# Performance work log

Measured on AMD Instinct MI355X. Metric: run time of the kernel, lower is better.

## Reference

```python
import jax, jax.numpy as jnp
import numpy as np

B, S, D, H = 2, 2048, 1024, 16
DK = D // H
NEG = -1.0e9

def setup_inputs() -> dict:
    key = jax.random.key(0)
    ks = jax.random.split(key, 12)
    sc = 1.0 / np.sqrt(D)
    q = jax.random.normal(ks[0], (B, S, D), jnp.float32)
    k = jax.random.normal(ks[1], (B, S, D), jnp.float32)
    v = jax.random.normal(ks[2], (B, S, D), jnp.float32)
    # causal mask: True = masked (matches masked_fill(mask == True, -1e9))
    mask = jnp.broadcast_to(jnp.triu(jnp.ones((S, S), bool), k=1)[None, None], (B, 1, S, S))
    Wq = jax.random.normal(ks[3], (D, D), jnp.float32) * sc
    bq = jnp.zeros((D,), jnp.float32)
    Wk = jax.random.normal(ks[4], (D, D), jnp.float32) * sc
    bk = jnp.zeros((D,), jnp.float32)
    Wv = jax.random.normal(ks[5], (D, D), jnp.float32) * sc
    bv = jnp.zeros((D,), jnp.float32)
    Wo = jax.random.normal(ks[6], (D, D), jnp.float32) * sc
    bo = jnp.zeros((D,), jnp.float32)
    return {"q": q, "k": k, "v": v, "mask": mask,
            "Wq": Wq, "bq": bq, "Wk": Wk, "bk": bk,
            "Wv": Wv, "bv": bv, "Wo": Wo, "bo": bo}

def reference(q, k, v, mask, Wq, bq, Wk, bk, Wv, bv, Wo, bo):
    def split_heads(x):  # [B,S,D] -> [B,H,S,DK]
        return x.reshape(B, S, H, DK).transpose(0, 2, 1, 3)
    qh = split_heads(q @ Wq + bq)
    kh = split_heads(k @ Wk + bk)
    vh = split_heads(v @ Wv + bv)
    scores = jnp.einsum('bhqd,bhkd->bhqk', qh, kh) / np.sqrt(DK)
    scores = jnp.where(mask, NEG, scores)
    p = jax.nn.softmax(scores, axis=-1)
    out = jnp.einsum('bhqk,bhkd->bhqd', p, vh)  # [B,H,S,DK]
    out = out.transpose(0, 2, 1, 3).reshape(B, S, D)
    return out @ Wo + bo
```

## Files before the change

### kernel.cpp

```cpp
#include <hip/hip_runtime.h>

#define BB 2
#define SS 2048
#define DD 1024
#define HH 16
#define DKK 64

typedef __attribute__((ext_vector_type(8))) short short8;
typedef __attribute__((ext_vector_type(4))) float floatx4;

__device__ inline float bf2f(ushort u) {
    union { unsigned int i; float f; } x; x.i = ((unsigned int)u) << 16; return x.f;
}
__device__ inline ushort f2bf(float f) {
    union { float f; unsigned int i; } x; x.f = f;
    unsigned int r = x.i + 0x7fff + ((x.i >> 16) & 1);
    return (ushort)(r >> 16);
}
__device__ inline void async_cp16(const ushort* g, ushort* l) {
    __builtin_amdgcn_global_load_lds(
        (const __attribute__((address_space(1))) unsigned int*)g,
        (__attribute__((address_space(3))) unsigned int*)l, 16, 0, 0);
}
__device__ inline unsigned int cvt_pk_bf16(float lo, float hi) {
    unsigned int r;
    asm("v_cvt_pk_bf16_f32 %0, %1, %2" : "=v"(r) : "v"(lo), "v"(hi));
    return r;
}
__device__ inline void swap32(unsigned int& a, unsigned int& b) {
    asm("v_permlane32_swap_b32 %0, %1" : "+v"(a), "+v"(b));
}
__device__ inline void swap16(unsigned int& a, unsigned int& b) {
    asm("v_permlane16_swap_b32 %0, %1" : "+v"(a), "+v"(b));
}

__global__ __launch_bounds__(256) void cvt_w4(const float* __restrict__ w0,
                                              const float* __restrict__ w1,
                                              const float* __restrict__ w2,
                                              const float* __restrict__ w3,
                                              ushort* __restrict__ o0,
                                              ushort* __restrict__ o1,
                                              ushort* __restrict__ o2,
                                              ushort* __restrict__ o3) {
    __shared__ ushort t[32][33];
    int z = blockIdx.z;
    const float* in = (z == 0) ? w0 : (z == 1) ? w1 : (z == 2) ? w2 : w3;
    ushort* out = (z == 0) ? o0 : (z == 1) ? o1 : (z == 2) ? o2 : o3;
    int bx = blockIdx.x, by = blockIdx.y, tx = threadIdx.x;
    for (int i = threadIdx.y; i < 32; i += 8)
        t[i][tx] = f2bf(in[(size_t)(by * 32 + i) * DD + bx * 32 + tx]);
    __syncthreads();
    for (int i = threadIdx.y; i < 32; i += 8)
        out[(size_t)(bx * 32 + i) * DD + by * 32 + tx] = t[tx][i];
}

__global__ __launch_bounds__(256) void cvt_qkv(const float* __restrict__ q,
                                               const float* __restrict__ k,
                                               const float* __restrict__ v,
                                               ushort* __restrict__ oq,
                                               ushort* __restrict__ ok,
                                               ushort* __restrict__ ov) {
    int z = blockIdx.z;
    const float* in = (z == 0) ? q : (z == 1) ? k : v;
    ushort* out = (z == 0) ? oq : (z == 1) ? ok : ov;
    int i = blockIdx.x * 256 + threadIdx.x;
    float4 f0 = ((const float4*)in)[i * 2];
    float4 f1 = ((const float4*)in)[i * 2 + 1];
    short8 p;
    p[0] = (short)f2bf(f0.x); p[1] = (short)f2bf(f0.y);
    p[2] = (short)f2bf(f0.z); p[3] = (short)f2bf(f0.w);
    p[4] = (short)f2bf(f1.x); p[5] = (short)f2bf(f1.y);
    p[6] = (short)f2bf(f1.z); p[7] = (short)f2bf(f1.w);
    ((short8*)out)[i] = p;
}

__global__ __launch_bounds__(512, 2) void gemm_qkv(const ushort* __restrict__ Xq,
                                                   const ushort* __restrict__ Xk,
                                                   const ushort* __restrict__ Xv,
                                                   const ushort* __restrict__ WtQ,
                                                   const ushort* __restrict__ WtK,
                                                   const ushort* __restrict__ WtV,
                                                   const float* __restrict__ bq,
                                                   const float* __restrict__ bk,
                                                   const float* __restrict__ bv,
                                                   ushort* __restrict__ qh,
                                                   ushort* __restrict__ kh,
                                                   ushort* __restrict__ vt) {
    constexpr int K = 1024;
    constexpr int NKT = 32;
    __shared__ ushort smem[32768];

    int lin = blockIdx.x + (blockIdx.y << 2) + (blockIdx.z << 6);
    int wid = (lin & 7) * 24 + (lin >> 3);
    int z = wid >> 6;
    int rem = wid & 63;
    int byy = rem >> 2, bxx = rem & 3;
    int rowBase = byy * 256, colBase = bxx * 256;

    const ushort* Ag = (z == 0) ? Xq : (z == 1) ? Xk : Xv;
    const ushort* Bg = (z == 0) ? WtQ : (z == 1) ? WtK : WtV;
    const float* bias = (z == 0) ? bq : (z == 1) ? bk : bv;
    ushort* outp = (z == 0) ? qh : (z == 1) ? kh : vt;

    int tid = threadIdx.x;
    int wave = tid >> 6, lane = tid & 63, quad = lane >> 4, l15 = lane & 15;
    int wm = wave >> 2, wn = wave & 3;

    size_t srcA[2], srcB[2];
    int dstU[2];
#pragma unroll
    for (int r = 0; r < 2; ++r) {
        int lb = r * 8192 + wave * 1024 + lane * 16;
        int sl = lb ^ (((lb >> 9) & 1) << 5);
        int srow = sl >> 6;
        int scol = (sl & 63) >> 1;
        srcA[r] = (size_t)(rowBase + srow) * K + scol;
        srcB[r] = (size_t)(colBase + srow) * K + scol;
        dstU[r] = r * 4096 + wave * 512;
    }
    int aOff[2][4], bOff[4];
#pragma unroll
    for (int mh = 0; mh < 2; ++mh)
#pragma unroll
        for (int mi = 0; mi < 4; ++mi) {
            int row = wm * 128 + mh * 64 + mi * 16 + l15;
            aOff[mh][mi] = row * 32 + ((quad * 8) ^ (((row >> 3) & 1) << 4));
        }
#pragma unroll
    for (int ni = 0; ni < 4; ++ni) {
        int row = wn * 64 + ni * 16 + l15;
        bOff[ni] = 8192 + row * 32 + ((quad * 8) ^ (((row >> 3) & 1) << 4));
    }

    auto stageTile = [&](int u) {
        int slot = (u & 1) << 14;
        const ushort* As = Ag + u * 32;
        const ushort* Bs = Bg + u * 32;
        async_cp16(As + srcA[0], &smem[slot + dstU[0]]);
        async_cp16(As + srcA[1], &smem[slot + dstU[1]]);
        async_cp16(Bs + srcB[0], &smem[slot + 8192 + dstU[0]]);
        async_cp16(Bs + srcB[1], &smem[slot + 8192 + dstU[1]]);
    };

    floatx4 acc[8][4] = {};
    stageTile(0);
    for (int t = 0; t < NKT; ++t) {
        if (t < NKT - 1) {
            stageTile(t + 1);
            asm volatile("s_waitcnt vmcnt(4)" ::: "memory");
        } else {
            asm volatile("s_waitcnt vmcnt(0)" ::: "memory");
        }
        __builtin_amdgcn_s_barrier();
        __builtin_amdgcn_sched_barrier(0);
        int slot = (t & 1) << 14;
        short8 bfr[4];
#pragma unroll
        for (int ni = 0; ni < 4; ++ni)
            bfr[ni] = *(const short8*)&smem[slot + bOff[ni]];
#pragma unroll
        for (int mh = 0; mh < 2; ++mh) {
            short8 af[4];
#pragma unroll
            for (int mi = 0; mi < 4; ++mi)
                af[mi] = *(const short8*)&smem[slot + aOff[mh][mi]];
#pragma unroll
            for (int mi = 0; mi < 4; ++mi)
#pragma unroll
                for (int ni = 0; ni < 4; ++ni)
                    acc[mh * 4 + mi][ni] = __builtin_amdgcn_mfma_f32_16x16x32_bf16(
                        af[mi], bfr[ni], acc[mh * 4 + mi][ni], 0, 0, 0);
        }
        __builtin_amdgcn_sched_barrier(0);
        __builtin_amdgcn_s_barrier();
    }

    float bvv[4];
#pragma unroll
    for (int ni = 0; ni < 4; ++ni)
        bvv[ni] = bias[colBase + wn * 64 + ni * 16 + l15];
    if (z == 2) {
#pragma unroll
        for (int mi = 0; mi < 8; ++mi)
#pragma unroll
            for (int ni = 0; ni < 4; ++ni) {
                int col = colBase + wn * 64 + ni * 16 + l15;
                int h = col >> 6, dk = col & 63;
                int rowg = rowBase + wm * 128 + mi * 16 + quad * 4;
                int b = rowg >> 11, s = rowg & 2047;
                int2 v;
                v.x = (int)cvt_pk_bf16(acc[mi][ni][0] + bvv[ni], acc[mi][ni][1] + bvv[ni]);
                v.y = (int)cvt_pk_bf16(acc[mi][ni][2] + bvv[ni], acc[mi][ni][3] + bvv[ni]);
                *(int2*)&outp[((size_t)((b * HH + h) * DKK + dk)) * SS + s] = v;
            }
    } else {
#pragma unroll
        for (int mi = 0; mi < 8; ++mi)
#pragma unroll
            for (int ni = 0; ni < 4; ++ni) {
                int col = colBase + wn * 64 + ni * 16 + l15;
                int h = col >> 6, dk = col & 63;
#pragma unroll
                for (int i = 0; i < 4; ++i) {
                    int rowg = rowBase + wm * 128 + mi * 16 + quad * 4 + i;
                    int b = rowg >> 11, s = rowg & 2047;
                    outp[((size_t)((b * HH + h) * SS + s)) * DKK + dk] =
                        f2bf(acc[mi][ni][i] + bvv[ni]);
                }
            }
    }
}

__global__ __launch_bounds__(256) void gemm_fin(const ushort* __restrict__ A,
                                                const ushort* __restrict__ Bt,
                                                const float* __restrict__ bias,
                                                float* __restrict__ outp) {
    constexpr int K = 1024, N = 1024, NT = 32;
    __shared__ ushort smem[12288];
    int tid = threadIdx.x;
    int wave = tid >> 6, lane = tid & 63, quad = lane >> 4, l15 = lane & 15;
    int wm = wave >> 1, wn = wave & 1;

    int lin = blockIdx.x + (blockIdx.y << 3);
    int wid = (lin & 7) * 64 + (lin >> 3);
    int bx = wid & 7, by = wid >> 3;
    int rowBase = by * 64, colBase = bx * 128;

    auto stage = [&](int k0, int d) {
        int ab = d * 6144, bb2 = 2048 + d * 6144;
#pragma unroll
        for (int j = 0; j < 3; ++j) {
            int c = j * 4 + wave;
            int cbase = (c < 4) ? c * 64 : (c - 4) * 64;
            int cc = cbase + lane;
            int row = cc >> 2, sub = (cc & 3) * 8;
            if (c < 4)
                async_cp16(&A[(size_t)(rowBase + row) * K + k0 + sub], &smem[ab + cbase * 8]);
            else
                async_cp16(&Bt[(size_t)(colBase + row) * K + k0 + sub], &smem[bb2 + cbase * 8]);
        }
    };

    floatx4 acc[2][4] = {};
    stage(0, 0);
    __syncthreads();
    for (int t = 0; t < NT; ++t) {
        if (t + 1 < NT) stage((t + 1) * 32, (t + 1) & 1);
        int ab = (t & 1) * 6144, bb2 = 2048 + (t & 1) * 6144;
        short8 af[2], bf[4];
#pragma unroll
        for (int mi = 0; mi < 2; ++mi)
            af[mi] = *(const short8*)&smem[ab + (wm * 32 + mi * 16 + l15) * 32 + quad * 8];
#pragma unroll
        for (int ni = 0; ni < 4; ++ni)
            bf[ni] = *(const short8*)&smem[bb2 + (wn * 64 + ni * 16 + l15) * 32 + quad * 8];
#pragma unroll
        for (int mi = 0; mi < 2; ++mi)
#pragma unroll
            for (int ni = 0; ni < 4; ++ni)
                acc[mi][ni] = __builtin_amdgcn_mfma_f32_16x16x32_bf16(
                    af[mi], bf[ni], acc[mi][ni], 0, 0, 0);
        __syncthreads();
    }
    for (int mi = 0; mi < 2; ++mi)
        for (int ni = 0; ni < 4; ++ni) {
            int col = colBase + wn * 64 + ni * 16 + l15;
            float bv = bias[col];
            for (int i = 0; i < 4; ++i) {
                int row = rowBase + wm * 32 + mi * 16 + quad * 4 + i;
                outp[(size_t)row * N + col] = acc[mi][ni][i] + bv;
            }
        }
}

__global__ __launch_bounds__(256, 2) void flash_attn5(const ushort* __restrict__ qh,
                                                      const ushort* __restrict__ kh,
                                                      const ushort* __restrict__ vt,
                                                      ushort* __restrict__ attn) {
    constexpr int LD = 72;
    __shared__ ushort Ksm[2][64 * LD];
    __shared__ ushort Vsm[2][64 * LD];
    int tid = threadIdx.x;
    int h = blockIdx.y, b = blockIdx.z;
    int wave = tid >> 6, lane = tid & 63, quad = lane >> 4, l15 = lane & 15;
    const size_t headQK = ((size_t)(b * HH + h)) * SS * DKK;
    const size_t headV  = ((size_t)(b * HH + h)) * DKK * SS;
    int c0 = tid, r0 = c0 >> 3, s0 = (c0 & 7) * 8;
    int c1 = tid + 256, r1 = c1 >> 3, s1 = (c1 & 7) * 8;
    const int qt0 = blockIdx.x;
    const int qt1 = 31 - qt0;

    int qrow0 = qt0 * 64 + wave * 16 + l15;
    int qrow1 = qt1 * 64 + wave * 16 + l15;
    short8 q0a = *(const short8*)&qh[headQK + (size_t)qrow0 * DKK + quad * 8];
    short8 q0b = *(const short8*)&qh[headQK + (size_t)qrow0 * DKK + 32 + quad * 8];
    short8 q1a = *(const short8*)&qh[headQK + (size_t)qrow1 * DKK + quad * 8];
    short8 q1b = *(const short8*)&qh[headQK + (size_t)qrow1 * DKK + 32 + quad * 8];

    floatx4 o0[4] = {}, o1[4] = {};
    float l0 = 0.f, l1 = 0.f;
    int qsel = wave * 16 + l15;

    *(int4*)&Ksm[0][r0 * LD + s0] = *(const int4*)&kh[headQK + (size_t)r0 * DKK + s0];
    *(int4*)&Ksm[0][r1 * LD + s1] = *(const int4*)&kh[headQK + (size_t)r1 * DKK + s1];
    *(int4*)&Vsm[0][r0 * LD + s0] = *(const int4*)&vt[headV + (size_t)r0 * SS + s0];
    *(int4*)&Vsm[0][r1 * LD + s1] = *(const int4*)&vt[headV + (size_t)r1 * SS + s1];
    __syncthreads();

    for (int kt = 0; kt <= qt1; ++kt) {
        int cur = kt & 1;
        bool pre = (kt < qt1);
        bool act0 = (kt <= qt0);
        int4 kA, kB, vA, vB;
        if (pre) {
            const ushort* kp = &kh[headQK + (size_t)((kt + 1) * 64) * DKK];
            const ushort* vp = &vt[headV + (kt + 1) * 64];
            kA = *(const int4*)&kp[(size_t)r0 * DKK + s0];
            kB = *(const int4*)&kp[(size_t)r1 * DKK + s1];
            vA = *(const int4*)&vp[(size_t)r0 * SS + s0];
            vB = *(const int4*)&vp[(size_t)r1 * SS + s1];
        }
        floatx4 sv1[4], sv0[4];
#pragma unroll
        for (int cn = 0; cn < 4; ++cn) {
            short8 kf0 = *(const short8*)&Ksm[cur][(cn * 16 + l15) * LD + quad * 8];
            short8 kf1 = *(const short8*)&Ksm[cur][(cn * 16 + l15) * LD + 32 + quad * 8];
            floatx4 zz = {};
            zz = __builtin_amdgcn_mfma_f32_16x16x32_bf16(kf0, q1a, zz, 0, 0, 0);
            zz = __builtin_amdgcn_mfma_f32_16x16x32_bf16(kf1, q1b, zz, 0, 0, 0);
            sv1[cn] = zz;
            if (act0) {
                floatx4 y = {};
                y = __builtin_amdgcn_mfma_f32_16x16x32_bf16(kf0, q0a, y, 0, 0, 0);
                y = __builtin_amdgcn_mfma_f32_16x16x32_bf16(kf1, q0b, y, 0, 0, 0);
                sv0[cn] = y;
            }
        }
        short8 vf[2][4];
#pragma unroll
        for (int ks = 0; ks < 2; ++ks)
#pragma unroll
            for (int n = 0; n < 4; ++n)
                vf[ks][n] = *(const short8*)&Vsm[cur][(n * 16 + l15) * LD + ks * 32 + quad * 8];

        {
            bool diag = (kt == qt1);
            unsigned int pkd[4][2];
#pragma unroll
            for (int cn = 0; cn < 4; ++cn) {
#pragma unroll
                for (int i = 0; i < 4; ++i) {
                    float p = __expf(sv1[cn][i] * 0.125f);
                    if (diag && (cn * 16 + quad * 4 + i) > qsel) p = 0.f;
                    sv1[cn][i] = p;
                    l1 += p;
                }
                pkd[cn][0] = cvt_pk_bf16(sv1[cn][0], sv1[cn][1]);
                pkd[cn][1] = cvt_pk_bf16(sv1[cn][2], sv1[cn][3]);
            }
#pragma unroll
            for (int ks = 0; ks < 2; ++ks) {
                unsigned int a0 = pkd[ks * 2][0], b0 = pkd[ks * 2 + 1][0];
                swap32(a0, b0); swap16(a0, b0);
                unsigned int a1 = pkd[ks * 2][1], b1 = pkd[ks * 2 + 1][1];
                swap32(a1, b1); swap16(a1, b1);
                union { int4 i4; short8 s8; } u;
                u.i4 = make_int4((int)a0, (int)a1, (int)b0, (int)b1);
#pragma unroll
                for (int n = 0; n < 4; ++n)
                    o1[n] = __builtin_amdgcn_mfma_f32_16x16x32_bf16(
                        vf[ks][n], u.s8, o1[n], 0, 0, 0);
            }
        }
        if (act0) {
            bool diag = (kt == qt0);
            unsigned int pkd[4][2];
#pragma unroll
            for (int cn = 0; cn < 4; ++cn) {
#pragma unroll
                for (int i = 0; i < 4; ++i) {
                    float p = __expf(sv0[cn][i] * 0.125f);
                    if (diag && (cn * 16 + quad * 4 + i) > qsel) p = 0.f;
                    sv0[cn][i] = p;
                    l0 += p;
                }
                pkd[cn][0] = cvt_pk_bf16(sv0[cn][0], sv0[cn][1]);
                pkd[cn][1] = cvt_pk_bf16(sv0[cn][2], sv0[cn][3]);
            }
#pragma unroll
            for (int ks = 0; ks < 2; ++ks) {
                unsigned int a0 = pkd[ks * 2][0], b0 = pkd[ks * 2 + 1][0];
                swap32(a0, b0); swap16(a0, b0);
                unsigned int a1 = pkd[ks * 2][1], b1 = pkd[ks * 2 + 1][1];
                swap32(a1, b1); swap16(a1, b1);
                union { int4 i4; short8 s8; } u;
                u.i4 = make_int4((int)a0, (int)a1, (int)b0, (int)b1);
#pragma unroll
                for (int n = 0; n < 4; ++n)
                    o0[n] = __builtin_amdgcn_mfma_f32_16x16x32_bf16(
                        vf[ks][n], u.s8, o0[n], 0, 0, 0);
            }
        }
        if (pre) {
            int nb = cur ^ 1;
            *(int4*)&Ksm[nb][r0 * LD + s0] = kA;
            *(int4*)&Ksm[nb][r1 * LD + s1] = kB;
            *(int4*)&Vsm[nb][r0 * LD + s0] = vA;
            *(int4*)&Vsm[nb][r1 * LD + s1] = vB;
        }
        __syncthreads();
    }
    l0 += __shfl_xor(l0, 16, 64); l0 += __shfl_xor(l0, 32, 64);
    l1 += __shfl_xor(l1, 16, 64); l1 += __shfl_xor(l1, 32, 64);
    float inv0 = 1.0f / l0, inv1 = 1.0f / l1;
    size_t rowOff0 = ((size_t)(b * SS + qt0 * 64 + wave * 16 + l15)) * DD + h * 64;
    size_t rowOff1 = ((size_t)(b * SS + qt1 * 64 + wave * 16 + l15)) * DD + h * 64;
#pragma unroll
    for (int n = 0; n < 4; ++n) {
        int dof = n * 16 + quad * 4;
        int2 v0, v1;
        v0.x = (int)cvt_pk_bf16(o0[n][0] * inv0, o0[n][1] * inv0);
        v0.y = (int)cvt_pk_bf16(o0[n][2] * inv0, o0[n][3] * inv0);
        v1.x = (int)cvt_pk_bf16(o1[n][0] * inv1, o1[n][1] * inv1);
        v1.y = (int)cvt_pk_bf16(o1[n][2] * inv1, o1[n][3] * inv1);
        *(int2*)&attn[rowOff0 + dof] = v0;
        *(int2*)&attn[rowOff1 + dof] = v1;
    }
}

extern "C" void kernel_launch(void* const* d_in, const int* in_sizes, int n_in,
                              void* d_out, int out_size, void* d_ws, size_t ws_size,
                              hipStream_t stream) {
    const float* q  = (const float*)d_in[0];
    const float* k  = (const float*)d_in[1];
    const float* v  = (const float*)d_in[2];
    const float* Wq = (const float*)d_in[4];
    const float* bq = (const float*)d_in[5];
    const float* Wk = (const float*)d_in[6];
    const float* bk = (const float*)d_in[7];
    const float* Wv = (const float*)d_in[8];
    const float* bv = (const float*)d_in[9];
    const float* Wo = (const float*)d_in[10];
    const float* bo = (const float*)d_in[11];

    ushort* ws   = (ushort*)d_ws;
    ushort* WtQ  = ws;
    ushort* WtK  = WtQ + (1u << 20);
    ushort* WtV  = WtK + (1u << 20);
    ushort* WtO  = WtV + (1u << 20);
    ushort* Xv   = WtO + (1u << 20);
    ushort* qh   = Xv + (4u << 20);
    ushort* kh   = qh + (4u << 20);
    ushort* vt   = kh + (4u << 20);
    ushort* Xq   = (ushort*)d_out;
    ushort* Xk   = Xq + (4u << 20);
    ushort* attn = Xv;

    cvt_w4<<<dim3(32, 32, 4), dim3(32, 8), 0, stream>>>(Wq, Wk, Wv, Wo,
                                                        WtQ, WtK, WtV, WtO);
    cvt_qkv<<<dim3(2048, 1, 3), 256, 0, stream>>>(q, k, v, Xq, Xk, Xv);

    gemm_qkv<<<dim3(4, 16, 3), 512, 0, stream>>>(Xq, Xk, Xv, WtQ, WtK, WtV,
                                                 bq, bk, bv, qh, kh, vt);

    flash_attn5<<<dim3(16, 16, 2), 256, 0, stream>>>(qh, kh, vt, attn);

    gemm_fin<<<dim3(8, 64), 256, 0, stream>>>(attn, WtO, bo, (float*)d_out);
}
```

Baseline: 241.6 us.

## Merge conversion kernels, remap attention block order, add MFMA wave priorities

The weight-transpose and activation-conversion kernels become a single launch, removing one kernel launch and its tail. The flash attention grid is remapped so consecutive workgroups come from different heads, batches and query tiles, which spreads load across XCDs and L2. s_setprio raises wave priority around the MFMA sections so matrix work gets issued ahead of other waves. The priority hints and the new block order could also interfere with the overlap of loads and compute.

```diff
diff --git a/kernel.cpp b/kernel.cpp
--- a/kernel.cpp
+++ b/kernel.cpp
@@ -34,44 +34,47 @@
     asm("v_permlane16_swap_b32 %0, %1" : "+v"(a), "+v"(b));
 }
 
-__global__ __launch_bounds__(256) void cvt_w4(const float* __restrict__ w0,
-                                              const float* __restrict__ w1,
-                                              const float* __restrict__ w2,
-                                              const float* __restrict__ w3,
-                                              ushort* __restrict__ o0,
-                                              ushort* __restrict__ o1,
-                                              ushort* __restrict__ o2,
-                                              ushort* __restrict__ o3) {
+__global__ __launch_bounds__(256) void cvt_all(const float* __restrict__ q,
+                                               const float* __restrict__ k,
+                                               const float* __restrict__ v,
+                                               const float* __restrict__ w0,
+                                               const float* __restrict__ w1,
+                                               const float* __restrict__ w2,
+                                               const float* __restrict__ w3,
+                                               ushort* __restrict__ oq,
+                                               ushort* __restrict__ ok,
+                                               ushort* __restrict__ ov,
+                                               ushort* __restrict__ t0,
+                                               ushort* __restrict__ t1,
+                                               ushort* __restrict__ t2,
+                                               ushort* __restrict__ t3) {
     __shared__ ushort t[32][33];
     int z = blockIdx.z;
-    const float* in = (z == 0) ? w0 : (z == 1) ? w1 : (z == 2) ? w2 : w3;
-    ushort* out = (z == 0) ? o0 : (z == 1) ? o1 : (z == 2) ? o2 : o3;
-    int bx = blockIdx.x, by = blockIdx.y, tx = threadIdx.x;
-    for (int i = threadIdx.y; i < 32; i += 8)
-        t[i][tx] = f2bf(in[(size_t)(by * 32 + i) * DD + bx * 32 + tx]);
-    __syncthreads();
-    for (int i = threadIdx.y; i < 32; i += 8)
-        out[(size_t)(bx * 32 + i) * DD + by * 32 + tx] = t[tx][i];
-}
-
-__global__ __launch_bounds__(256) void cvt_qkv(const float* __restrict__ q,
-                                               const float* __restrict__ k,
-                                               const float* __restrict__ v,
-                                               ushort* __restrict__ oq,
-                                               ushort* __restrict__ ok,
-                                               ushort* __restrict__ ov) {
-    int z = blockIdx.z;
-    const float* in = (z == 0) ? q : (z == 1) ? k : v;
-    ushort* out = (z == 0) ? oq : (z == 1) ? ok : ov;
-    int i = blockIdx.x * 256 + threadIdx.x;
-    float4 f0 = ((const float4*)in)[i * 2];
-    float4 f1 = ((const float4*)in)[i * 2 + 1];
-    short8 p;
-    p[0] = (short)f2bf(f0.x); p[1] = (short)f2bf(f0.y);
-    p[2] = (short)f2bf(f0.z); p[3] = (short)f2bf(f0.w);
-    p[4] = (short)f2bf(f1.x); p[5] = (short)f2bf(f1.y);
-    p[6] = (short)f2bf(f1.z); p[7] = (short)f2bf(f1.w);
-    ((short8*)out)[i] = p;
+    if (z < 3) {
+        const float* in = (z == 0) ? q : (z == 1) ? k : v;
+        ushort* out = (z == 0) ? oq : (z == 1) ? ok : ov;
+        int i = blockIdx.x * 256 + threadIdx.x;
+        float4 f0 = ((const float4*)in)[i * 2];
+        float4 f1 = ((const float4*)in)[i * 2 + 1];
+        short8 p;
+        p[0] = (short)f2bf(f0.x); p[1] = (short)f2bf(f0.y);
+        p[2] = (short)f2bf(f0.z); p[3] = (short)f2bf(f0.w);
+        p[4] = (short)f2bf(f1.x); p[5] = (short)f2bf(f1.y);
+        p[6] = (short)f2bf(f1.z); p[7] = (short)f2bf(f1.w);
+        ((short8*)out)[i] = p;
+    } else {
+        int m = (z - 3) * 2 + (blockIdx.x >> 10);
+        int tile = blockIdx.x & 1023;
+        int bx = tile & 31, by = tile >> 5;
+        const float* in = (m == 0) ? w0 : (m == 1) ? w1 : (m == 2) ? w2 : w3;
+        ushort* out = (m == 0) ? t0 : (m == 1) ? t1 : (m == 2) ? t2 : t3;
+        int tx = threadIdx.x & 31, ty = threadIdx.x >> 5;
+        for (int i = ty; i < 32; i += 8)
+            t[i][tx] = f2bf(in[(size_t)(by * 32 + i) * DD + bx * 32 + tx]);
+        __syncthreads();
+        for (int i = ty; i < 32; i += 8)
+            out[(size_t)(bx * 32 + i) * DD + by * 32 + tx] = t[tx][i];
+    }
 }
 
 __global__ __launch_bounds__(512, 2) void gemm_qkv(const ushort* __restrict__ Xq,
@@ -281,14 +284,19 @@
     __shared__ ushort Ksm[2][64 * LD];
     __shared__ ushort Vsm[2][64 * LD];
     int tid = threadIdx.x;
-    int h = blockIdx.y, b = blockIdx.z;
     int wave = tid >> 6, lane = tid & 63, quad = lane >> 4, l15 = lane & 15;
+
+    int lin = blockIdx.x + (blockIdx.y << 4) + (blockIdx.z << 8);
+    int wid = (lin & 7) * 64 + (lin >> 3);
+    const int qt0 = wid & 15;
+    int h = (wid >> 4) & 15;
+    int b = wid >> 8;
+    const int qt1 = 31 - qt0;
+
     const size_t headQK = ((size_t)(b * HH + h)) * SS * DKK;
     const size_t headV  = ((size_t)(b * HH + h)) * DKK * SS;
     int c0 = tid, r0 = c0 >> 3, s0 = (c0 & 7) * 8;
     int c1 = tid + 256, r1 = c1 >> 3, s1 = (c1 & 7) * 8;
-    const int qt0 = blockIdx.x;
-    const int qt1 = 31 - qt0;
 
     int qrow0 = qt0 * 64 + wave * 16 + l15;
     int qrow1 = qt1 * 64 + wave * 16 + l15;
@@ -321,6 +329,7 @@
             vB = *(const int4*)&vp[(size_t)r1 * SS + s1];
         }
         floatx4 sv1[4], sv0[4];
+        __builtin_amdgcn_s_setprio(1);
 #pragma unroll
         for (int cn = 0; cn < 4; ++cn) {
             short8 kf0 = *(const short8*)&Ksm[cur][(cn * 16 + l15) * LD + quad * 8];
@@ -336,6 +345,7 @@
                 sv0[cn] = y;
             }
         }
+        __builtin_amdgcn_s_setprio(0);
         short8 vf[2][4];
 #pragma unroll
         for (int ks = 0; ks < 2; ++ks)
@@ -358,6 +368,7 @@
                 pkd[cn][0] = cvt_pk_bf16(sv1[cn][0], sv1[cn][1]);
                 pkd[cn][1] = cvt_pk_bf16(sv1[cn][2], sv1[cn][3]);
             }
+            __builtin_amdgcn_s_setprio(1);
 #pragma unroll
             for (int ks = 0; ks < 2; ++ks) {
                 unsigned int a0 = pkd[ks * 2][0], b0 = pkd[ks * 2 + 1][0];
@@ -371,6 +382,7 @@
                     o1[n] = __builtin_amdgcn_mfma_f32_16x16x32_bf16(
                         vf[ks][n], u.s8, o1[n], 0, 0, 0);
             }
+            __builtin_amdgcn_s_setprio(0);
         }
         if (act0) {
             bool diag = (kt == qt0);
@@ -387,6 +399,7 @@
                 pkd[cn][0] = cvt_pk_bf16(sv0[cn][0], sv0[cn][1]);
                 pkd[cn][1] = cvt_pk_bf16(sv0[cn][2], sv0[cn][3]);
             }
+            __builtin_amdgcn_s_setprio(1);
 #pragma unroll
             for (int ks = 0; ks < 2; ++ks) {
                 unsigned int a0 = pkd[ks * 2][0], b0 = pkd[ks * 2 + 1][0];
@@ -400,6 +413,7 @@
                     o0[n] = __builtin_amdgcn_mfma_f32_16x16x32_bf16(
                         vf[ks][n], u.s8, o0[n], 0, 0, 0);
             }
+            __builtin_amdgcn_s_setprio(0);
         }
         if (pre) {
             int nb = cur ^ 1;
@@ -456,9 +470,9 @@
     ushort* Xk   = Xq + (4u << 20);
     ushort* attn = Xv;
 
-    cvt_w4<<<dim3(32, 32, 4), dim3(32, 8), 0, stream>>>(Wq, Wk, Wv, Wo,
-                                                        WtQ, WtK, WtV, WtO);
-    cvt_qkv<<<dim3(2048, 1, 3), 256, 0, stream>>>(q, k, v, Xq, Xk, Xv);
+    cvt_all<<<dim3(2048, 1, 5), 256, 0, stream>>>(q, k, v, Wq, Wk, Wv, Wo,
+                                                  Xq, Xk, Xv,
+                                                  WtQ, WtK, WtV, WtO);
 
     gemm_qkv<<<dim3(4, 16, 3), 512, 0, stream>>>(Xq, Xk, Xv, WtQ, WtK, WtV,
                                                  bq, bk, bv, qh, kh, vt);
```

Measured after the change: 233.9 us. -3.2%, faster.
